# Kernel tuning notes

Measured on AMD Instinct MI355X. Metric: run time of the kernel, lower is better.

Reference implementation:

```python
import jax, jax.numpy as jnp
import numpy as np

EPS = 1e-10
NUM_RELATION = 4
N_NODES = 50000
N_EDGES = 800000
D_IN = 128
D_H = 256


def rgc_layer(x, src, dst, rel, rel_w, rel_b, loop_w, loop_b):
    # torchdrug RelationalGraphConv: scatter-mean per (node, relation), then
    # linear over concatenated per-relation features + self-loop linear + relu.
    N, d = x.shape
    msg = x[src]                                      # [E, d] gather
    idx = dst * NUM_RELATION + rel                    # [E] bucket per (node, relation)
    num_seg = N * NUM_RELATION
    agg = jax.ops.segment_sum(msg, idx, num_segments=num_seg)            # [N*R, d]
    cnt = jax.ops.segment_sum(jnp.ones((msg.shape[0], 1), x.dtype), idx,
                              num_segments=num_seg)                       # [N*R, 1]
    update = (agg / (cnt + EPS)).reshape(N, NUM_RELATION * d)            # [N, R*d]
    out = update @ rel_w + rel_b + x @ loop_w + loop_b                   # [N, d_out]
    return jax.nn.relu(out)


def highway(x, hp_w, hp_b, ht_w, ht_b):
    proj = jax.nn.relu(x @ hp_w + hp_b)
    gate = jax.nn.sigmoid(x @ ht_w + ht_b)
    return gate * proj + (1.0 - gate) * x


def setup_inputs() -> dict:
    key = jax.random.key(0)
    ks = jax.random.split(key, 16)
    s = 0.02
    inp = {
        "x": jax.random.normal(ks[0], (N_NODES, D_IN), dtype=jnp.float32),
        "src": jax.random.randint(ks[1], (N_EDGES,), 0, N_NODES, dtype=jnp.int32),
        "dst": jax.random.randint(ks[2], (N_EDGES,), 0, N_NODES, dtype=jnp.int32),
        "rel": jax.random.randint(ks[3], (N_EDGES,), 0, NUM_RELATION, dtype=jnp.int32),
        # layer 1: RGC(128->256) + Highway(256)
        "rel_w1": jax.random.normal(ks[4], (NUM_RELATION * D_IN, D_H), dtype=jnp.float32) * s,
        "rel_b1": jnp.zeros((D_H,), jnp.float32),
        "loop_w1": jax.random.normal(ks[5], (D_IN, D_H), dtype=jnp.float32) * s,
        "loop_b1": jnp.zeros((D_H,), jnp.float32),
        "hp_w1": jax.random.normal(ks[6], (D_H, D_H), dtype=jnp.float32) * s,
        "hp_b1": jnp.zeros((D_H,), jnp.float32),
        "ht_w1": jax.random.normal(ks[7], (D_H, D_H), dtype=jnp.float32) * s,
        "ht_b1": jnp.full((D_H,), -2.0, jnp.float32),  # transform.bias.data.fill_(-2.0)
        # layer 2: RGC(256->256) + Highway(256)
        "rel_w2": jax.random.normal(ks[8], (NUM_RELATION * D_H, D_H), dtype=jnp.float32) * s,
        "rel_b2": jnp.zeros((D_H,), jnp.float32),
        "loop_w2": jax.random.normal(ks[9], (D_H, D_H), dtype=jnp.float32) * s,
        "loop_b2": jnp.zeros((D_H,), jnp.float32),
        "hp_w2": jax.random.normal(ks[10], (D_H, D_H), dtype=jnp.float32) * s,
        "hp_b2": jnp.zeros((D_H,), jnp.float32),
        "ht_w2": jax.random.normal(ks[11], (D_H, D_H), dtype=jnp.float32) * s,
        "ht_b2": jnp.full((D_H,), -2.0, jnp.float32),
    }
    return inp


def reference(x, src, dst, rel,
              rel_w1, rel_b1, loop_w1, loop_b1, hp_w1, hp_b1, ht_w1, ht_b1,
              rel_w2, rel_b2, loop_w2, loop_b2, hp_w2, hp_b2, ht_w2, ht_b2):
    h = rgc_layer(x, src, dst, rel, rel_w1, rel_b1, loop_w1, loop_b1)
    h = highway(h, hp_w1, hp_b1, ht_w1, ht_b1)
    h = rgc_layer(h, src, dst, rel, rel_w2, rel_b2, loop_w2, loop_b2)
    h = highway(h, hp_w2, hp_b2, ht_w2, ht_b2)
    return h  # node_feature, shape [N, 256]
```

## Files before the change

kernel.cpp:

```cpp
#include <hip/hip_runtime.h>

typedef __bf16 bf16_t;
typedef __bf16 bf16x8 __attribute__((ext_vector_type(8)));
typedef __bf16 bf16x4 __attribute__((ext_vector_type(4)));
typedef float f32x4 __attribute__((ext_vector_type(4)));

#define BM 128
#define BN 128
#define BK 64

__device__ __forceinline__ void gload_lds16(const void* g, void* s) {
    __builtin_amdgcn_global_load_lds(
        (const __attribute__((address_space(1))) unsigned int*)g,
        (__attribute__((address_space(3))) unsigned int*)s, 16, 0, 0);
}

__global__ __launch_bounds__(256) void gemm_k(
    const bf16_t* __restrict__ A, int lda, int M,
    const bf16_t* __restrict__ Bt, int K,
    const float* __restrict__ bias, int relu_flag,
    bf16_t* __restrict__ outb, int ldo, int ocol,
    int NTM, int NTN)
{
    __shared__ __align__(16) bf16_t As[BM * BK];
    __shared__ __align__(16) bf16_t Bs[BN * BK];

    const int L    = blockIdx.x;
    const int xcd  = L & 7;
    const int rest = L >> 3;
    const int nt   = rest % NTN;
    const int sup  = rest / NTN;
    const int mt   = sup * 8 + xcd;
    if (mt >= NTM) return;
    const int m0 = mt * BM;
    const int n0 = nt * BN;

    const int tid  = threadIdx.x;
    const int wave = tid >> 6, lane = tid & 63;
    const int wr   = wave >> 1, wc = wave & 1;
    const int lm   = lane & 15, quad = lane >> 4;

    const bf16_t* ag[4];
    const bf16_t* bg[4];
    #pragma unroll
    for (int j = 0; j < 4; j++) {
        int c    = wave * 256 + j * 64 + lane;
        int row  = c >> 3;
        int cc   = (c & 7) ^ (row & 7);
        int col  = cc << 3;
        int gm   = m0 + row; if (gm >= M) gm = M - 1;
        ag[j] = A  + (size_t)gm * lda + col;
        bg[j] = Bt + (size_t)(n0 + row) * K + col;
    }

    f32x4 acc[4][4] = {};

    for (int k0 = 0; k0 < K; k0 += BK) {
        __syncthreads();
        #pragma unroll
        for (int j = 0; j < 4; j++)
            gload_lds16(ag[j] + k0, As + (size_t)(wave * 256 + j * 64) * 8);
        #pragma unroll
        for (int j = 0; j < 4; j++)
            gload_lds16(bg[j] + k0, Bs + (size_t)(wave * 256 + j * 64) * 8);
        __syncthreads();

        #pragma unroll
        for (int h = 0; h < 2; h++) {
            bf16x8 af[4], bfr[4];
            #pragma unroll
            for (int i = 0; i < 4; i++) {
                int r = wr * 64 + i * 16 + lm;
                af[i] = *(const bf16x8*)&As[(size_t)(r * 8 + ((h * 4 + quad) ^ (r & 7))) * 8];
            }
            #pragma unroll
            for (int i = 0; i < 4; i++) {
                int r = wc * 64 + i * 16 + lm;
                bfr[i] = *(const bf16x8*)&Bs[(size_t)(r * 8 + ((h * 4 + quad) ^ (r & 7))) * 8];
            }
            #pragma unroll
            for (int mi = 0; mi < 4; mi++)
                #pragma unroll
                for (int ni = 0; ni < 4; ni++)
                    acc[mi][ni] = __builtin_amdgcn_mfma_f32_16x16x32_bf16(
                        af[mi], bfr[ni], acc[mi][ni], 0, 0, 0);
        }
    }

    #pragma unroll
    for (int mi = 0; mi < 4; mi++) {
        #pragma unroll
        for (int ni = 0; ni < 4; ni++) {
            int col = n0 + wc * 64 + ni * 16 + lm;
            float b = bias[col];
            #pragma unroll
            for (int r = 0; r < 4; r++) {
                int row = m0 + wr * 64 + mi * 16 + quad * 4 + r;
                if (row < M) {
                    float v = acc[mi][ni][r] + b;
                    if (relu_flag) v = fmaxf(v, 0.f);
                    outb[(size_t)row * ldo + ocol + col] = (bf16_t)v;
                }
            }
        }
    }
}

__global__ __launch_bounds__(256) void gemm_hw2(
    const bf16_t* __restrict__ A, int M,
    const bf16_t* __restrict__ Bt,
    const float* __restrict__ bias,
    bf16_t* __restrict__ outb, int ldo, int ocol,
    float* __restrict__ outf, int NTM)
{
    __shared__ __align__(16) bf16_t As[128 * 64];
    __shared__ __align__(16) bf16_t Bs[128 * 64];

    const int L    = blockIdx.x;
    const int xcd  = L & 7;
    const int rest = L >> 3;
    const int nt   = rest % 4;
    const int sup  = rest / 4;
    const int mt   = sup * 8 + xcd;
    if (mt >= NTM) return;
    const int m0 = mt * 128;

    const int tid  = threadIdx.x;
    const int wave = tid >> 6, lane = tid & 63;
    const int lm   = lane & 15, quad = lane >> 4;

    const bf16_t* ag[4];
    const bf16_t* bg[4];
    #pragma unroll
    for (int j = 0; j < 4; j++) {
        int c    = wave * 256 + j * 64 + lane;
        int row  = c >> 3;
        int cc   = (c & 7) ^ (row & 7);
        int col  = cc << 3;
        int gm   = m0 + row; if (gm >= M) gm = M - 1;
        ag[j] = A + (size_t)gm * 256 + col;
        int grow = nt * 64 + row + ((row >= 64) ? 192 : 0);
        bg[j] = Bt + (size_t)grow * 256 + col;
    }

    f32x4 acc[2][8] = {};

    for (int k0 = 0; k0 < 256; k0 += 64) {
        __syncthreads();
        #pragma unroll
        for (int j = 0; j < 4; j++)
            gload_lds16(ag[j] + k0, As + (size_t)(wave * 256 + j * 64) * 8);
        #pragma unroll
        for (int j = 0; j < 4; j++)
            gload_lds16(bg[j] + k0, Bs + (size_t)(wave * 256 + j * 64) * 8);
        __syncthreads();

        #pragma unroll
        for (int h = 0; h < 2; h++) {
            bf16x8 af[2], bfr[8];
            #pragma unroll
            for (int i = 0; i < 2; i++) {
                int r = wave * 32 + i * 16 + lm;
                af[i] = *(const bf16x8*)&As[(size_t)(r * 8 + ((h * 4 + quad) ^ (r & 7))) * 8];
            }
            #pragma unroll
            for (int i = 0; i < 8; i++) {
                int r = i * 16 + lm;
                bfr[i] = *(const bf16x8*)&Bs[(size_t)(r * 8 + ((h * 4 + quad) ^ (r & 7))) * 8];
            }
            #pragma unroll
            for (int mi = 0; mi < 2; mi++)
                #pragma unroll
                for (int ni = 0; ni < 8; ni++)
                    acc[mi][ni] = __builtin_amdgcn_mfma_f32_16x16x32_bf16(
                        af[mi], bfr[ni], acc[mi][ni], 0, 0, 0);
        }
    }

    #pragma unroll
    for (int mi = 0; mi < 2; mi++) {
        #pragma unroll
        for (int ni = 0; ni < 4; ni++) {
            int col = nt * 64 + ni * 16 + lm;
            float bp = bias[col];
            float bg2 = bias[256 + col];
            #pragma unroll
            for (int r = 0; r < 4; r++) {
                int row = m0 + wave * 32 + mi * 16 + quad * 4 + r;
                if (row < M) {
                    float p = acc[mi][ni][r] + bp;
                    float g = acc[mi][ni + 4][r] + bg2;
                    float s = 1.0f / (1.0f + __expf(-g));
                    float hv = (float)A[(size_t)row * 256 + col];
                    float v = s * fmaxf(p, 0.f) + (1.0f - s) * hv;
                    if (outf) outf[(size_t)row * 256 + col] = v;
                    else      outb[(size_t)row * ldo + ocol + col] = (bf16_t)v;
                }
            }
        }
    }
}

__global__ void count_k(const int* __restrict__ dst, const int* __restrict__ rel,
                        int* __restrict__ cnt, int E)
{
    int e = blockIdx.x * blockDim.x + threadIdx.x;
    if (e < E) atomicAdd(&cnt[dst[e] * 4 + rel[e]], 1);
}

__global__ void scan_partial(const int* __restrict__ cnt, int* __restrict__ offs,
                             int* __restrict__ chunkSums, int NSEG)
{
    __shared__ int sh[256];
    int t = threadIdx.x;
    int idx = blockIdx.x * 256 + t;
    int v = (idx < NSEG) ? cnt[idx] : 0;
    sh[t] = v;
    __syncthreads();
    for (int d = 1; d < 256; d <<= 1) {
        int add = (t >= d) ? sh[t - d] : 0;
        __syncthreads();
        sh[t] += add;
        __syncthreads();
    }
    if (idx < NSEG) offs[idx] = sh[t] - v;
    if (t == 255) chunkSums[blockIdx.x] = sh[t];
}

__global__ void scan_chunks(int* __restrict__ chunkSums, int NCHUNK)
{
    __shared__ int sh[1024];
    int t = threadIdx.x;
    int v = (t < NCHUNK) ? chunkSums[t] : 0;
    sh[t] = v;
    __syncthreads();
    for (int d = 1; d < 1024; d <<= 1) {
        int add = (t >= d) ? sh[t - d] : 0;
        __syncthreads();
        sh[t] += add;
        __syncthreads();
    }
    if (t < NCHUNK) chunkSums[t] = sh[t] - v;
}

__global__ void scan_add(int* __restrict__ offs, const int* __restrict__ chunkSums,
                         int* __restrict__ cursor, int NSEG)
{
    int idx = blockIdx.x * 256 + threadIdx.x;
    if (idx < NSEG) {
        int o = offs[idx] + chunkSums[blockIdx.x];
        offs[idx] = o;
        cursor[idx] = o;
    }
}

__global__ void fill_k(const int* __restrict__ src, const int* __restrict__ dst,
                       const int* __restrict__ rel,
                       int* __restrict__ cursor, int* __restrict__ eidx, int E)
{
    int e = blockIdx.x * blockDim.x + threadIdx.x;
    if (e < E) {
        int seg = dst[e] * 4 + rel[e];
        int pos = atomicAdd(&cursor[seg], 1);
        eidx[pos] = src[e];
    }
}

__global__ void seg_mean256(const int* __restrict__ offs, const int* __restrict__ cnt,
                            const int* __restrict__ eidx,
                            const bf16_t* __restrict__ xb, int ldx,
                            bf16_t* __restrict__ Aout, int lda, int NSEG)
{
    int wv = (blockIdx.x << 2) + (threadIdx.x >> 6);
    if (wv >= NSEG) return;
    int lane = threadIdx.x & 63;
    int half = lane >> 5;
    int c = (lane & 31) << 3;
    int start = offs[wv];
    int n = cnt[wv];
    float acc[8] = {};
    int i = 0;
    for (; i + 8 <= n; i += 8) {
        int s0 = eidx[start + i + 0 + half];
        int s1 = eidx[start + i + 2 + half];
        int s2 = eidx[start + i + 4 + half];
        int s3 = eidx[start + i + 6 + half];
        bf16x8 v0 = *(const bf16x8*)(xb + (size_t)s0 * ldx + c);
        bf16x8 v1 = *(const bf16x8*)(xb + (size_t)s1 * ldx + c);
        bf16x8 v2 = *(const bf16x8*)(xb + (size_t)s2 * ldx + c);
        bf16x8 v3 = *(const bf16x8*)(xb + (size_t)s3 * ldx + c);
        #pragma unroll
        for (int j = 0; j < 8; j++)
            acc[j] += ((float)v0[j] + (float)v1[j]) + ((float)v2[j] + (float)v3[j]);
    }
    for (; i + 2 <= n; i += 2) {
        int s = eidx[start + i + half];
        bf16x8 v = *(const bf16x8*)(xb + (size_t)s * ldx + c);
        #pragma unroll
        for (int j = 0; j < 8; j++) acc[j] += (float)v[j];
    }
    if (i < n && half == 0) {
        int s = eidx[start + i];
        bf16x8 v = *(const bf16x8*)(xb + (size_t)s * ldx + c);
        #pragma unroll
        for (int j = 0; j < 8; j++) acc[j] += (float)v[j];
    }
    #pragma unroll
    for (int j = 0; j < 8; j++) acc[j] += __shfl_xor(acc[j], 32, 64);
    if (half == 0) {
        float inv = 1.0f / ((float)n + 1e-10f);
        int node = wv >> 2, r = wv & 3;
        bf16x8 o;
        #pragma unroll
        for (int j = 0; j < 8; j++) o[j] = (bf16_t)(acc[j] * inv);
        *(bf16x8*)(Aout + (size_t)node * lda + r * 256 + c) = o;
    }
}

__global__ void seg_mean128(const int* __restrict__ offs, const int* __restrict__ cnt,
                            const int* __restrict__ eidx,
                            const bf16_t* __restrict__ xb, int ldx,
                            bf16_t* __restrict__ Aout, int lda, int NSEG)
{
    int wv = (blockIdx.x << 2) + (threadIdx.x >> 6);
    if (wv >= NSEG) return;
    int lane = threadIdx.x & 63;
    int q = lane >> 4;
    int c = (lane & 15) << 3;
    int start = offs[wv];
    int n = cnt[wv];
    float acc[8] = {};
    int i = 0;
    for (; i + 8 <= n; i += 8) {
        int s0 = eidx[start + i + q];
        int s1 = eidx[start + i + 4 + q];
        bf16x8 v0 = *(const bf16x8*)(xb + (size_t)s0 * ldx + c);
        bf16x8 v1 = *(const bf16x8*)(xb + (size_t)s1 * ldx + c);
        #pragma unroll
        for (int j = 0; j < 8; j++) acc[j] += (float)v0[j] + (float)v1[j];
    }
    for (; i + 4 <= n; i += 4) {
        int s = eidx[start + i + q];
        bf16x8 v = *(const bf16x8*)(xb + (size_t)s * ldx + c);
        #pragma unroll
        for (int j = 0; j < 8; j++) acc[j] += (float)v[j];
    }
    if (q < n - i) {
        int s = eidx[start + i + q];
        bf16x8 v = *(const bf16x8*)(xb + (size_t)s * ldx + c);
        #pragma unroll
        for (int j = 0; j < 8; j++) acc[j] += (float)v[j];
    }
    #pragma unroll
    for (int j = 0; j < 8; j++) {
        acc[j] += __shfl_xor(acc[j], 16, 64);
        acc[j] += __shfl_xor(acc[j], 32, 64);
    }
    if (lane < 16) {
        float inv = 1.0f / ((float)n + 1e-10f);
        int node = wv >> 2, r = wv & 3;
        bf16x8 o;
        #pragma unroll
        for (int j = 0; j < 8; j++) o[j] = (bf16_t)(acc[j] * inv);
        *(bf16x8*)(Aout + (size_t)node * lda + r * 128 + c) = o;
    }
}

__global__ void convert_x_k(const float* __restrict__ x, bf16_t* __restrict__ A1, int N)
{
    int t = blockIdx.x * blockDim.x + threadIdx.x;
    if (t >= N * 32) return;
    int row = t >> 5;
    int c = (t & 31) << 2;
    f32x4 v = *(const f32x4*)(x + (size_t)row * 128 + c);
    bf16x4 o;
    o[0] = (bf16_t)v[0]; o[1] = (bf16_t)v[1]; o[2] = (bf16_t)v[2]; o[3] = (bf16_t)v[3];
    *(bf16x4*)(A1 + (size_t)row * 640 + 512 + c) = o;
}

__global__ void transpose_w(const float* __restrict__ W, bf16_t* __restrict__ Wt,
                            int K, int ldk, int k0, int n0)
{
    int t = blockIdx.x * blockDim.x + threadIdx.x;
    if (t >= K * 256) return;
    int k = t >> 8, n = t & 255;
    Wt[(size_t)(n0 + n) * ldk + k0 + k] = (bf16_t)W[(size_t)k * 256 + n];
}

__global__ void prep_bias(const float* rb1, const float* lb1,
                          const float* rb2, const float* lb2,
                          const float* hpb1, const float* htb1,
                          const float* hpb2, const float* htb2,
                          float* bR1, float* bR2, float* bH1, float* bH2)
{
    int t = threadIdx.x;
    bR1[t] = rb1[t] + lb1[t];
    bR2[t] = rb2[t] + lb2[t];
    bH1[t] = hpb1[t]; bH1[256 + t] = htb1[t];
    bH2[t] = hpb2[t]; bH2[256 + t] = htb2[t];
}

extern "C" void kernel_launch(void* const* d_in, const int* in_sizes, int n_in,
                              void* d_out, int out_size, void* d_ws, size_t ws_size,
                              hipStream_t stream)
{
    const float* x       = (const float*)d_in[0];
    const int*   src     = (const int*)d_in[1];
    const int*   dst     = (const int*)d_in[2];
    const int*   rel     = (const int*)d_in[3];
    const float* rel_w1  = (const float*)d_in[4];
    const float* rel_b1  = (const float*)d_in[5];
    const float* loop_w1 = (const float*)d_in[6];
    const float* loop_b1 = (const float*)d_in[7];
    const float* hp_w1   = (const float*)d_in[8];
    const float* hp_b1   = (const float*)d_in[9];
    const float* ht_w1   = (const float*)d_in[10];
    const float* ht_b1   = (const float*)d_in[11];
    const float* rel_w2  = (const float*)d_in[12];
    const float* rel_b2  = (const float*)d_in[13];
    const float* loop_w2 = (const float*)d_in[14];
    const float* loop_b2 = (const float*)d_in[15];
    const float* hp_w2   = (const float*)d_in[16];
    const float* hp_b2   = (const float*)d_in[17];
    const float* ht_w2   = (const float*)d_in[18];
    const float* ht_b2   = (const float*)d_in[19];

    const int N = in_sizes[0] / 128;
    const int E = in_sizes[1];
    const int NSEG = N * 4;
    const int NCHUNK = (NSEG + 255) / 256;
    float* out = (float*)d_out;

    char* ws = (char*)d_ws;
    size_t off = 0;
    auto alloc = [&](size_t bytes) {
        void* p = ws + off;
        off += (bytes + 255) & ~(size_t)255;
        return p;
    };
    int*    cnt    = (int*)alloc((size_t)NSEG * 4);
    int*    offs   = (int*)alloc((size_t)NSEG * 4);
    int*    cursor = (int*)alloc((size_t)NSEG * 4);
    int*    chunkS = (int*)alloc(4096);
    int*    eidx   = (int*)alloc((size_t)E * 4);
    bf16_t* A1     = (bf16_t*)alloc((size_t)N * 640 * 2);
    bf16_t* A2     = (bf16_t*)alloc((size_t)N * 1280 * 2);
    bf16_t* h      = (bf16_t*)alloc((size_t)N * 256 * 2);
    bf16_t* W1t    = (bf16_t*)alloc((size_t)256 * 640 * 2);
    bf16_t* W2t    = (bf16_t*)alloc((size_t)256 * 1280 * 2);
    bf16_t* Wh1t   = (bf16_t*)alloc((size_t)512 * 256 * 2);
    bf16_t* Wh2t   = (bf16_t*)alloc((size_t)512 * 256 * 2);
    float*  bR1    = (float*)alloc(256 * 4);
    float*  bR2    = (float*)alloc(256 * 4);
    float*  bH1    = (float*)alloc(512 * 4);
    float*  bH2    = (float*)alloc(512 * 4);

    dim3 blk(256);
    const int NTM = (N + BM - 1) / BM;
    const int supers = (NTM + 7) / 8;
    const int gridRGC = supers * 8 * 2;
    const int gridHW  = supers * 8 * 4;

    transpose_w<<<dim3(512), blk, 0, stream>>>(rel_w1, W1t, 512, 640, 0, 0);
    transpose_w<<<dim3(128), blk, 0, stream>>>(loop_w1, W1t, 128, 640, 512, 0);
    transpose_w<<<dim3(1024), blk, 0, stream>>>(rel_w2, W2t, 1024, 1280, 0, 0);
    transpose_w<<<dim3(256), blk, 0, stream>>>(loop_w2, W2t, 256, 1280, 1024, 0);
    transpose_w<<<dim3(256), blk, 0, stream>>>(hp_w1, Wh1t, 256, 256, 0, 0);
    transpose_w<<<dim3(256), blk, 0, stream>>>(ht_w1, Wh1t, 256, 256, 0, 256);
    transpose_w<<<dim3(256), blk, 0, stream>>>(hp_w2, Wh2t, 256, 256, 0, 0);
    transpose_w<<<dim3(256), blk, 0, stream>>>(ht_w2, Wh2t, 256, 256, 0, 256);
    prep_bias<<<dim3(1), blk, 0, stream>>>(rel_b1, loop_b1, rel_b2, loop_b2,
                                           hp_b1, ht_b1, hp_b2, ht_b2,
                                           bR1, bR2, bH1, bH2);
    convert_x_k<<<dim3((N * 32 + 255) / 256), blk, 0, stream>>>(x, A1, N);

    hipMemsetAsync(cnt, 0, (size_t)NSEG * 4, stream);
    count_k<<<dim3((E + 255) / 256), blk, 0, stream>>>(dst, rel, cnt, E);
    scan_partial<<<dim3(NCHUNK), blk, 0, stream>>>(cnt, offs, chunkS, NSEG);
    scan_chunks<<<dim3(1), dim3(1024), 0, stream>>>(chunkS, NCHUNK);
    scan_add<<<dim3(NCHUNK), blk, 0, stream>>>(offs, chunkS, cursor, NSEG);
    fill_k<<<dim3((E + 255) / 256), blk, 0, stream>>>(src, dst, rel, cursor, eidx, E);

    seg_mean128<<<dim3((NSEG + 3) / 4), blk, 0, stream>>>(offs, cnt, eidx,
                                                          A1 + 512, 640, A1, 640, NSEG);
    gemm_k<<<dim3(gridRGC), blk, 0, stream>>>(A1, 640, N, W1t, 640,
                                              bR1, 1, h, 256, 0, NTM, 2);
    gemm_hw2<<<dim3(gridHW), blk, 0, stream>>>(h, N, Wh1t, bH1,
                                               A2, 1280, 1024, nullptr, NTM);

    seg_mean256<<<dim3((NSEG + 3) / 4), blk, 0, stream>>>(offs, cnt, eidx,
                                                          A2 + 1024, 1280, A2, 1280, NSEG);
    gemm_k<<<dim3(gridRGC), blk, 0, stream>>>(A2, 1280, N, W2t, 1280,
                                              bR2, 1, h, 256, 0, NTM, 2);
    gemm_hw2<<<dim3(gridHW), blk, 0, stream>>>(h, N, Wh2t, bH2,
                                               nullptr, 0, 0, out, NTM);
}
```

Before: 553.5 us.

## Widen GEMM tiles to full N width and fuse prep kernels into one launch

The RGC GEMM now computes a 128x256 tile per block, covering the whole output width, so each A tile is loaded once instead of twice. The highway GEMM now uses 2 N-tiles of 128 (proj plus gate) instead of 4 of 64, which halves the number of A reloads. Both GEMMs get launch_bounds with a minimum of 2 blocks and larger LDS and register footprints. The weight transposes, bias prep, x conversion and the cnt memset are merged into a single prep_all launch to cut launch overhead, at the cost of fewer blocks in flight and more accumulator registers per wave.

```diff
diff --git a/kernel.cpp b/kernel.cpp
--- a/kernel.cpp
+++ b/kernel.cpp
@@ -4,9 +4,9 @@
 typedef __bf16 bf16x8 __attribute__((ext_vector_type(8)));
 typedef __bf16 bf16x4 __attribute__((ext_vector_type(4)));
 typedef float f32x4 __attribute__((ext_vector_type(4)));
+typedef int i32x4 __attribute__((ext_vector_type(4)));
 
 #define BM 128
-#define BN 128
 #define BK 64
 
 __device__ __forceinline__ void gload_lds16(const void* g, void* s) {
@@ -15,25 +15,22 @@
         (__attribute__((address_space(3))) unsigned int*)s, 16, 0, 0);
 }
 
-__global__ __launch_bounds__(256) void gemm_k(
+__global__ __launch_bounds__(256, 2) void gemm_k(
     const bf16_t* __restrict__ A, int lda, int M,
     const bf16_t* __restrict__ Bt, int K,
     const float* __restrict__ bias, int relu_flag,
     bf16_t* __restrict__ outb, int ldo, int ocol,
-    int NTM, int NTN)
+    int NTM)
 {
     __shared__ __align__(16) bf16_t As[BM * BK];
-    __shared__ __align__(16) bf16_t Bs[BN * BK];
-
-    const int L    = blockIdx.x;
-    const int xcd  = L & 7;
-    const int rest = L >> 3;
-    const int nt   = rest % NTN;
-    const int sup  = rest / NTN;
-    const int mt   = sup * 8 + xcd;
+    __shared__ __align__(16) bf16_t Bs[256 * BK];
+
+    const int L   = blockIdx.x;
+    const int xcd = L & 7;
+    const int sup = L >> 3;
+    const int mt  = sup * 8 + xcd;
     if (mt >= NTM) return;
     const int m0 = mt * BM;
-    const int n0 = nt * BN;
 
     const int tid  = threadIdx.x;
     const int wave = tid >> 6, lane = tid & 63;
@@ -41,57 +38,60 @@
     const int lm   = lane & 15, quad = lane >> 4;
 
     const bf16_t* ag[4];
-    const bf16_t* bg[4];
+    const bf16_t* bg[8];
     #pragma unroll
     for (int j = 0; j < 4; j++) {
-        int c    = wave * 256 + j * 64 + lane;
-        int row  = c >> 3;
-        int cc   = (c & 7) ^ (row & 7);
-        int col  = cc << 3;
-        int gm   = m0 + row; if (gm >= M) gm = M - 1;
-        ag[j] = A  + (size_t)gm * lda + col;
-        bg[j] = Bt + (size_t)(n0 + row) * K + col;
-    }
-
-    f32x4 acc[4][4] = {};
+        int c   = j * 256 + tid;
+        int row = c >> 3;
+        int col = ((c & 7) ^ (row & 7)) << 3;
+        int gm  = m0 + row; if (gm >= M) gm = M - 1;
+        ag[j] = A + (size_t)gm * lda + col;
+    }
+    #pragma unroll
+    for (int j = 0; j < 8; j++) {
+        int c   = j * 256 + tid;
+        int row = c >> 3;
+        int col = ((c & 7) ^ (row & 7)) << 3;
+        bg[j] = Bt + (size_t)row * K + col;
+    }
+
+    f32x4 acc[4][8] = {};
 
     for (int k0 = 0; k0 < K; k0 += BK) {
         __syncthreads();
         #pragma unroll
         for (int j = 0; j < 4; j++)
-            gload_lds16(ag[j] + k0, As + (size_t)(wave * 256 + j * 64) * 8);
-        #pragma unroll
-        for (int j = 0; j < 4; j++)
-            gload_lds16(bg[j] + k0, Bs + (size_t)(wave * 256 + j * 64) * 8);
+            gload_lds16(ag[j] + k0, As + (size_t)(j * 256 + tid) * 8);
+        #pragma unroll
+        for (int j = 0; j < 8; j++)
+            gload_lds16(bg[j] + k0, Bs + (size_t)(j * 256 + tid) * 8);
         __syncthreads();
 
         #pragma unroll
         for (int h = 0; h < 2; h++) {
-            bf16x8 af[4], bfr[4];
+            bf16x8 af[4];
             #pragma unroll
             for (int i = 0; i < 4; i++) {
                 int r = wr * 64 + i * 16 + lm;
                 af[i] = *(const bf16x8*)&As[(size_t)(r * 8 + ((h * 4 + quad) ^ (r & 7))) * 8];
             }
             #pragma unroll
-            for (int i = 0; i < 4; i++) {
-                int r = wc * 64 + i * 16 + lm;
-                bfr[i] = *(const bf16x8*)&Bs[(size_t)(r * 8 + ((h * 4 + quad) ^ (r & 7))) * 8];
+            for (int ni = 0; ni < 8; ni++) {
+                int r = wc * 128 + ni * 16 + lm;
+                bf16x8 bfr = *(const bf16x8*)&Bs[(size_t)(r * 8 + ((h * 4 + quad) ^ (r & 7))) * 8];
+                #pragma unroll
+                for (int mi = 0; mi < 4; mi++)
+                    acc[mi][ni] = __builtin_amdgcn_mfma_f32_16x16x32_bf16(
+                        af[mi], bfr, acc[mi][ni], 0, 0, 0);
             }
-            #pragma unroll
-            for (int mi = 0; mi < 4; mi++)
-                #pragma unroll
-                for (int ni = 0; ni < 4; ni++)
-                    acc[mi][ni] = __builtin_amdgcn_mfma_f32_16x16x32_bf16(
-                        af[mi], bfr[ni], acc[mi][ni], 0, 0, 0);
         }
     }
 
     #pragma unroll
     for (int mi = 0; mi < 4; mi++) {
         #pragma unroll
-        for (int ni = 0; ni < 4; ni++) {
-            int col = n0 + wc * 64 + ni * 16 + lm;
+        for (int ni = 0; ni < 8; ni++) {
+            int col = wc * 128 + ni * 16 + lm;
             float b = bias[col];
             #pragma unroll
             for (int r = 0; r < 4; r++) {
@@ -106,7 +106,7 @@
     }
 }
 
-__global__ __launch_bounds__(256) void gemm_hw2(
+__global__ __launch_bounds__(256, 2) void gemm_hw2(
     const bf16_t* __restrict__ A, int M,
     const bf16_t* __restrict__ Bt,
     const float* __restrict__ bias,
@@ -114,13 +114,13 @@
     float* __restrict__ outf, int NTM)
 {
     __shared__ __align__(16) bf16_t As[128 * 64];
-    __shared__ __align__(16) bf16_t Bs[128 * 64];
+    __shared__ __align__(16) bf16_t Bs[256 * 64];
 
     const int L    = blockIdx.x;
     const int xcd  = L & 7;
     const int rest = L >> 3;
-    const int nt   = rest % 4;
-    const int sup  = rest / 4;
+    const int nt   = rest & 1;
+    const int sup  = rest >> 1;
     const int mt   = sup * 8 + xcd;
     if (mt >= NTM) return;
     const int m0 = mt * 128;
@@ -130,66 +130,69 @@
     const int lm   = lane & 15, quad = lane >> 4;
 
     const bf16_t* ag[4];
-    const bf16_t* bg[4];
+    const bf16_t* bg[8];
     #pragma unroll
     for (int j = 0; j < 4; j++) {
-        int c    = wave * 256 + j * 64 + lane;
+        int c   = j * 256 + tid;
+        int row = c >> 3;
+        int col = ((c & 7) ^ (row & 7)) << 3;
+        int gm  = m0 + row; if (gm >= M) gm = M - 1;
+        ag[j] = A + (size_t)gm * 256 + col;
+    }
+    #pragma unroll
+    for (int j = 0; j < 8; j++) {
+        int c    = j * 256 + tid;
         int row  = c >> 3;
-        int cc   = (c & 7) ^ (row & 7);
-        int col  = cc << 3;
-        int gm   = m0 + row; if (gm >= M) gm = M - 1;
-        ag[j] = A + (size_t)gm * 256 + col;
-        int grow = nt * 64 + row + ((row >= 64) ? 192 : 0);
+        int col  = ((c & 7) ^ (row & 7)) << 3;
+        int grow = nt * 128 + row + ((row >= 128) ? 128 : 0);
         bg[j] = Bt + (size_t)grow * 256 + col;
     }
 
-    f32x4 acc[2][8] = {};
+    f32x4 acc[2][16] = {};
 
     for (int k0 = 0; k0 < 256; k0 += 64) {
         __syncthreads();
         #pragma unroll
         for (int j = 0; j < 4; j++)
-            gload_lds16(ag[j] + k0, As + (size_t)(wave * 256 + j * 64) * 8);
-        #pragma unroll
-        for (int j = 0; j < 4; j++)
-            gload_lds16(bg[j] + k0, Bs + (size_t)(wave * 256 + j * 64) * 8);
+            gload_lds16(ag[j] + k0, As + (size_t)(j * 256 + tid) * 8);
+        #pragma unroll
+        for (int j = 0; j < 8; j++)
+            gload_lds16(bg[j] + k0, Bs + (size_t)(j * 256 + tid) * 8);
         __syncthreads();
 
         #pragma unroll
         for (int h = 0; h < 2; h++) {
-            bf16x8 af[2], bfr[8];
+            bf16x8 af[2];
             #pragma unroll
             for (int i = 0; i < 2; i++) {
                 int r = wave * 32 + i * 16 + lm;
                 af[i] = *(const bf16x8*)&As[(size_t)(r * 8 + ((h * 4 + quad) ^ (r & 7))) * 8];
             }
             #pragma unroll
-            for (int i = 0; i < 8; i++) {
-                int r = i * 16 + lm;
-                bfr[i] = *(const bf16x8*)&Bs[(size_t)(r * 8 + ((h * 4 + quad) ^ (r & 7))) * 8];
+            for (int ni = 0; ni < 16; ni++) {
+                int r = ni * 16 + lm;
+                bf16x8 bfr = *(const bf16x8*)&Bs[(size_t)(r * 8 + ((h * 4 + quad) ^ (r & 7))) * 8];
+                #pragma unroll
+                for (int mi = 0; mi < 2; mi++)
+                    acc[mi][ni] = __builtin_amdgcn_mfma_f32_16x16x32_bf16(
+                        af[mi], bfr, acc[mi][ni], 0, 0, 0);
             }
-            #pragma unroll
-            for (int mi = 0; mi < 2; mi++)
-                #pragma unroll
-                for (int ni = 0; ni < 8; ni++)
-                    acc[mi][ni] = __builtin_amdgcn_mfma_f32_16x16x32_bf16(
-                        af[mi], bfr[ni], acc[mi][ni], 0, 0, 0);
         }
     }
 
     #pragma unroll
     for (int mi = 0; mi < 2; mi++) {
         #pragma unroll
-        for (int ni = 0; ni < 4; ni++) {
-            int col = nt * 64 + ni * 16 + lm;
-            float bp = bias[col];
+        for (int ni = 0; ni < 8; ni++) {
+            int col = nt * 128 + ni * 16 + lm;
+            float bp  = bias[col];
             float bg2 = bias[256 + col];
             #pragma unroll
             for (int r = 0; r < 4; r++) {
                 int row = m0 + wave * 32 + mi * 16 + quad * 4 + r;
                 if (row < M) {
                     float p = acc[mi][ni][r] + bp;
-                    float g = acc[mi][ni + 4][r] + bg2;
+                    float g = acc[mi][ni + 8][r] + bg2;
                     float s = 1.0f / (1.0f + __expf(-g));
                     float hv = (float)A[(size_t)row * 256 + col];
                     float v = s * fmaxf(p, 0.f) + (1.0f - s) * hv;
@@ -197,6 +200,60 @@
                     else      outb[(size_t)row * ldo + ocol + col] = (bf16_t)v;
                 }
             }
+        }
+    }
+}
+
+__global__ void prep_all(
+    const float* __restrict__ rel_w1, const float* __restrict__ loop_w1,
+    const float* __restrict__ rel_w2, const float* __restrict__ loop_w2,
+    const float* __restrict__ hp_w1,  const float* __restrict__ ht_w1,
+    const float* __restrict__ hp_w2,  const float* __restrict__ ht_w2,
+    bf16_t* __restrict__ W1t, bf16_t* __restrict__ W2t,
+    bf16_t* __restrict__ Wh1t, bf16_t* __restrict__ Wh2t,
+    const float* __restrict__ rb1, const float* __restrict__ lb1,
+    const float* __restrict__ rb2, const float* __restrict__ lb2,
+    const float* __restrict__ hpb1, const float* __restrict__ htb1,
+    const float* __restrict__ hpb2, const float* __restrict__ htb2,
+    float* __restrict__ bR1, float* __restrict__ bR2,
+    float* __restrict__ bH1, float* __restrict__ bH2,
+    const float* __restrict__ x, bf16_t* __restrict__ A1, int N,
+    int* __restrict__ cnt, int NSEG, int cvb)
+{
+    int b = blockIdx.x, tid = threadIdx.x;
+    if (b < 2944) {
+        const float* W; bf16_t* Wt; int ldk, k0, n0, base;
+        if      (b < 512)  { W = rel_w1;  Wt = W1t;  ldk = 640;  k0 = 0;    n0 = 0;   base = 0; }
+        else if (b < 640)  { W = loop_w1; Wt = W1t;  ldk = 640;  k0 = 512;  n0 = 0;   base = 512; }
+        else if (b < 1664) { W = rel_w2;  Wt = W2t;  ldk = 1280; k0 = 0;    n0 = 0;   base = 640; }
+        else if (b < 1920) { W = loop_w2; Wt = W2t;  ldk = 1280; k0 = 1024; n0 = 0;   base = 1664; }
+        else if (b < 2176) { W = hp_w1;   Wt = Wh1t; ldk = 256;  k0 = 0;    n0 = 0;   base = 1920; }
+        else if (b < 2432) { W = ht_w1;   Wt = Wh1t; ldk = 256;  k0 = 0;    n0 = 256; base = 2176; }
+        else if (b < 2688) { W = hp_w2;   Wt = Wh2t; ldk = 256;  k0 = 0;    n0 = 0;   base = 2432; }
+        else               { W = ht_w2;   Wt = Wh2t; ldk = 256;  k0 = 0;    n0 = 256; base = 2688; }
+        int k = b - base;
+        int n = tid;
+        Wt[(size_t)(n0 + n) * ldk + k0 + k] = (bf16_t)W[(size_t)k * 256 + n];
+    } else if (b == 2944) {
+        int t = tid;
+        bR1[t] = rb1[t] + lb1[t];
+        bR2[t] = rb2[t] + lb2[t];
+        bH1[t] = hpb1[t]; bH1[256 + t] = htb1[t];
+        bH2[t] = hpb2[t]; bH2[256 + t] = htb2[t];
+    } else if (b < 2945 + cvb) {
+        int t = (b - 2945) * 256 + tid;
+        if (t < N * 32) {
+            int row = t >> 5, c = (t & 31) << 2;
+            f32x4 v = *(const f32x4*)(x + (size_t)row * 128 + c);
+            bf16x4 o;
+            o[0] = (bf16_t)v[0]; o[1] = (bf16_t)v[1]; o[2] = (bf16_t)v[2]; o[3] = (bf16_t)v[3];
+            *(bf16x4*)(A1 + (size_t)row * 640 + 512 + c) = o;
+        }
+    } else {
+        int t = ((b - 2945 - cvb) * 256 + tid) * 4;
+        if (t < NSEG) {
+            i32x4 z = {0, 0, 0, 0};
+            *(i32x4*)(cnt + t) = z;
         }
     }
 }
@@ -364,40 +421,6 @@
         for (int j = 0; j < 8; j++) o[j] = (bf16_t)(acc[j] * inv);
         *(bf16x8*)(Aout + (size_t)node * lda + r * 128 + c) = o;
     }
-}
-
-__global__ void convert_x_k(const float* __restrict__ x, bf16_t* __restrict__ A1, int N)
-{
-    int t = blockIdx.x * blockDim.x + threadIdx.x;
-    if (t >= N * 32) return;
-    int row = t >> 5;
-    int c = (t & 31) << 2;
-    f32x4 v = *(const f32x4*)(x + (size_t)row * 128 + c);
-    bf16x4 o;
-    o[0] = (bf16_t)v[0]; o[1] = (bf16_t)v[1]; o[2] = (bf16_t)v[2]; o[3] = (bf16_t)v[3];
-    *(bf16x4*)(A1 + (size_t)row * 640 + 512 + c) = o;
-}
-
-__global__ void transpose_w(const float* __restrict__ W, bf16_t* __restrict__ Wt,
-                            int K, int ldk, int k0, int n0)
-{
-    int t = blockIdx.x * blockDim.x + threadIdx.x;
-    if (t >= K * 256) return;
-    int k = t >> 8, n = t & 255;
-    Wt[(size_t)(n0 + n) * ldk + k0 + k] = (bf16_t)W[(size_t)k * 256 + n];
-}
-
-__global__ void prep_bias(const float* rb1, const float* lb1,
-                          const float* rb2, const float* lb2,
-                          const float* hpb1, const float* htb1,
-                          const float* hpb2, const float* htb2,
-                          float* bR1, float* bR2, float* bH1, float* bH2)
-{
-    int t = threadIdx.x;
-    bR1[t] = rb1[t] + lb1[t];
-    bR2[t] = rb2[t] + lb2[t];
-    bH1[t] = hpb1[t]; bH1[256 + t] = htb1[t];
-    bH2[t] = hpb2[t]; bH2[256 + t] = htb2[t];
 }
 
 extern "C" void kernel_launch(void* const* d_in, const int* in_sizes, int n_in,
@@ -458,23 +481,18 @@
     dim3 blk(256);
     const int NTM = (N + BM - 1) / BM;
     const int supers = (NTM + 7) / 8;
-    const int gridRGC = supers * 8 * 2;
-    const int gridHW  = supers * 8 * 4;
-
-    transpose_w<<<dim3(512), blk, 0, stream>>>(rel_w1, W1t, 512, 640, 0, 0);
-    transpose_w<<<dim3(128), blk, 0, stream>>>(loop_w1, W1t, 128, 640, 512, 0);
-    transpose_w<<<dim3(1024), blk, 0, stream>>>(rel_w2, W2t, 1024, 1280, 0, 0);
-    transpose_w<<<dim3(256), blk, 0, stream>>>(loop_w2, W2t, 256, 1280, 1024, 0);
-    transpose_w<<<dim3(256), blk, 0, stream>>>(hp_w1, Wh1t, 256, 256, 0, 0);
-    transpose_w<<<dim3(256), blk, 0, stream>>>(ht_w1, Wh1t, 256, 256, 0, 256);
-    transpose_w<<<dim3(256), blk, 0, stream>>>(hp_w2, Wh2t, 256, 256, 0, 0);
-    transpose_w<<<dim3(256), blk, 0, stream>>>(ht_w2, Wh2t, 256, 256, 0, 256);
-    prep_bias<<<dim3(1), blk, 0, stream>>>(rel_b1, loop_b1, rel_b2, loop_b2,
-                                           hp_b1, ht_b1, hp_b2, ht_b2,
-                                           bR1, bR2, bH1, bH2);
-    convert_x_k<<<dim3((N * 32 + 255) / 256), blk, 0, stream>>>(x, A1, N);
-
-    hipMemsetAsync(cnt, 0, (size_t)NSEG * 4, stream);
+    const int gridRGC = supers * 8;
+    const int gridHW  = supers * 8 * 2;
+
+    const int cvb = (N * 32 + 255) / 256;
+    const int zb  = (NSEG / 4 + 255) / 256;
+    prep_all<<<dim3(2945 + cvb + zb), blk, 0, stream>>>(
+        rel_w1, loop_w1, rel_w2, loop_w2, hp_w1, ht_w1, hp_w2, ht_w2,
+        W1t, W2t, Wh1t, Wh2t,
+        rel_b1, loop_b1, rel_b2, loop_b2, hp_b1, ht_b1, hp_b2, ht_b2,
+        bR1, bR2, bH1, bH2,
+        x, A1, N, cnt, NSEG, cvb);
+
     count_k<<<dim3((E + 255) / 256), blk, 0, stream>>>(dst, rel, cnt, E);
     scan_partial<<<dim3(NCHUNK), blk, 0, stream>>>(cnt, offs, chunkS, NSEG);
     scan_chunks<<<dim3(1), dim3(1024), 0, stream>>>(chunkS, NCHUNK);
@@ -484,14 +502,14 @@
     seg_mean128<<<dim3((NSEG + 3) / 4), blk, 0, stream>>>(offs, cnt, eidx,
                                                           A1 + 512, 640, A1, 640, NSEG);
     gemm_k<<<dim3(gridRGC), blk, 0, stream>>>(A1, 640, N, W1t, 640,
-                                              bR1, 1, h, 256, 0, NTM, 2);
+                                              bR1, 1, h, 256, 0, NTM);
     gemm_hw2<<<dim3(gridHW), blk, 0, stream>>>(h, N, Wh1t, bH1,
                                                A2, 1280, 1024, nullptr, NTM);
 
     seg_mean256<<<dim3((NSEG + 3) / 4), blk, 0, stream>>>(offs, cnt, eidx,
                                                           A2 + 1024, 1280, A2, 1280, NSEG);
     gemm_k<<<dim3(gridRGC), blk, 0, stream>>>(A2, 1280, N, W2t, 1280,
-                                              bR2, 1, h, 256, 0, NTM, 2);
+                                              bR2, 1, h, 256, 0, NTM);
     gemm_hw2<<<dim3(gridHW), blk, 0, stream>>>(h, N, Wh2t, bH2,
                                                nullptr, 0, 0, out, NTM);
 }
```

Result: faster. 513.8 us, median of 3 (-7.2%).
